# Performance work log

Measured on AMD Instinct MI355X. Metric: run time of the kernel, lower is better.

## Reference

```python
import jax, jax.numpy as jnp
import numpy as np

N_QUBITS = 8
DEPTH = 2
INPUT_DIM = 128
HIDDEN_DIM = 256
SEQ_LEN = 64
BATCH = 128
DIM = 2 ** N_QUBITS


def _rx(t):
    c = jnp.cos(0.5 * t).astype(jnp.complex64)
    s = (-1j * jnp.sin(0.5 * t)).astype(jnp.complex64)
    return jnp.stack([jnp.stack([c, s], -1), jnp.stack([s, c], -1)], -2)


def _ry(t):
    c = jnp.cos(0.5 * t).astype(jnp.complex64)
    s = jnp.sin(0.5 * t).astype(jnp.complex64)
    return jnp.stack([jnp.stack([c, -s], -1), jnp.stack([s, c], -1)], -2)


def _rz(t):
    e0 = jnp.exp(-0.5j * t).astype(jnp.complex64)
    e1 = jnp.exp(0.5j * t).astype(jnp.complex64)
    z = jnp.zeros_like(e0)
    return jnp.stack([jnp.stack([e0, z], -1), jnp.stack([z, e1], -1)], -2)


def _apply_1q(state, U, q):
    # state: (B, 2**n) complex; U: (2,2) shared or (B,2,2) per-sample
    b = state.shape[0]
    s = state.reshape(b, 2 ** q, 2, -1)
    if U.ndim == 2:
        s = jnp.einsum('ij,bljr->blir', U, s)
    else:
        s = jnp.einsum('bij,bljr->blir', U, s)
    return s.reshape(b, DIM)


def _apply_cnot(state, c, t):
    b = state.shape[0]
    s = state.reshape((b,) + (2,) * N_QUBITS)
    ac, at = 1 + c, 1 + t
    s0 = jnp.take(s, 0, axis=ac)
    s1 = jnp.take(s, 1, axis=ac)
    at2 = at - 1 if at > ac else at  # target axis shifts after slicing control axis
    s1 = jnp.flip(s1, axis=at2)
    s = jnp.stack([s0, s1], axis=ac)
    return s.reshape(b, DIM)


def _quantum_gate(x, params):
    # x: (B, n_qubits) data angles; params: (n_qubits, depth, 3) RX/RY/RZ angles
    b = x.shape[0]
    state = jnp.zeros((b, DIM), jnp.complex64).at[:, 0].set(1.0)
    for q in range(N_QUBITS):
        state = _apply_1q(state, _rx(x[:, q]), q)
    for d in range(DEPTH):
        for q in range(N_QUBITS):
            state = _apply_1q(state, _rx(params[q, d, 0]), q)
            state = _apply_1q(state, _ry(params[q, d, 1]), q)
            state = _apply_1q(state, _rz(params[q, d, 2]), q)
        for q in range(N_QUBITS - 1):
            state = _apply_cnot(state, q, q + 1)
        state = _apply_cnot(state, N_QUBITS - 1, 0)
    probs = state.real ** 2 + state.imag ** 2
    outs = []
    for q in range(N_QUBITS):  # <Z_q> = P(q=0) - P(q=1)
        p = probs.reshape(b, 2 ** q, 2, -1)
        outs.append(p[:, :, 0, :].sum((1, 2)) - p[:, :, 1, :].sum((1, 2)))
    return jnp.stack(outs, axis=1)


def _qlstm(inputs, Wf, bf, qf, Uf, cf, Wi, bi, qi, Ui, ci, Wg, bg, qg, Ug, cg, Wo, bo, qo, Uo, co):
    B = inputs.shape[1]
    h0 = jnp.zeros((B, HIDDEN_DIM), inputs.dtype)
    c0 = jnp.zeros((B, HIDDEN_DIM), inputs.dtype)

    def step(carry, x):
        hx, cx = carry
        comb = jnp.concatenate([x, hx], axis=1)

        def gate(W, b_, qp, U, c_):
            return _quantum_gate(comb @ W.T + b_, qp) @ U.T + c_

        f = jax.nn.sigmoid(gate(Wf, bf, qf, Uf, cf))
        i = jax.nn.sigmoid(gate(Wi, bi, qi, Ui, ci))
        g = jnp.tanh(gate(Wg, bg, qg, Ug, cg))
        o = jax.nn.sigmoid(gate(Wo, bo, qo, Uo, co))
        cx2 = f * cx + i * g
        hx2 = o * jnp.tanh(cx2)
        return (hx2, cx2), hx2

    (hx, cx), stacked = jax.lax.scan(step, (h0, c0), inputs)
    return stacked, hx, cx


def setup_inputs() -> dict:
    key = jax.random.key(0)
    ks = jax.random.split(key, 16)
    d = INPUT_DIM + HIDDEN_DIM
    inp = {"inputs": jax.random.normal(ks[0], (SEQ_LEN, BATCH, INPUT_DIM), jnp.float32)}
    k = 1
    for n in ("f", "i", "g", "o"):
        inp["W" + n] = jax.random.normal(ks[k], (N_QUBITS, d), jnp.float32) * 0.05; k += 1
        inp["b" + n] = jnp.zeros((N_QUBITS,), jnp.float32)
        inp["q" + n] = jax.random.normal(ks[k], (N_QUBITS, DEPTH, 3), jnp.float32) * 0.1; k += 1
        inp["U" + n] = jax.random.normal(ks[k], (HIDDEN_DIM, N_QUBITS), jnp.float32) * 0.05; k += 1
        inp["c" + n] = jnp.zeros((HIDDEN_DIM,), jnp.float32)
    return inp


def reference(inputs, Wf, bf, qf, Uf, cf, Wi, bi, qi, Ui, ci, Wg, bg, qg, Ug, cg, Wo, bo, qo, Uo, co):
    stacked, hx, cx = _qlstm(inputs, Wf, bf, qf, Uf, cf, Wi, bi, qi, Ui, ci,
                             Wg, bg, qg, Ug, cg, Wo, bo, qo, Uo, co)
    return stacked, (hx, cx)
```

## Files before the change

### kernel.cpp

```cpp
#include <hip/hip_runtime.h>
#include <math.h>

#define BB   128
#define TT   64
#define IND  128
#define HID  256
#define CD   384

struct C2 { float x, y; };
__device__ __forceinline__ C2 cmul(C2 a, C2 b) { return {a.x*b.x - a.y*b.y, a.x*b.y + a.y*b.x}; }
__device__ __forceinline__ C2 cadd(C2 a, C2 b) { return {a.x + b.x, a.y + b.y}; }
__device__ __forceinline__ C2 csub(C2 a, C2 b) { return {a.x - b.x, a.y - b.y}; }
__device__ __forceinline__ C2 conjc(C2 a) { return {a.x, -a.y}; }

struct Args {
    const float* x;
    const float* W[4];
    const float* bb[4];
    const float* qp[4];
    const float* Uo[4];
    const float* cb[4];
    float* out;
};

template<int CTRL>
__device__ __forceinline__ int dppmv(int v) {
    return __builtin_amdgcn_update_dpp(v, v, CTRL, 0xF, 0xF, false);
}

template<int M>
__device__ __forceinline__ float lx(float v) {
    int i = __float_as_int(v);
    if constexpr (M == 1)
        return __int_as_float(dppmv<0xB1>(i));
    else if constexpr (M == 2)
        return __int_as_float(dppmv<0x4E>(i));
    else if constexpr (M == 4) {
        int a = dppmv<0x104>(i);
        int b = dppmv<0x114>(i);
        return __int_as_float((threadIdx.x & 4) ? b : a);
    } else if constexpr (M == 8)
        return __int_as_float(dppmv<0x128>(i));
    else if constexpr (M == 16) {
#if __has_builtin(__builtin_amdgcn_permlane16_swap)
        auto r = __builtin_amdgcn_permlane16_swap(i, i, false, false);
        return __int_as_float((threadIdx.x & 16) ? r[0] : r[1]);
#else
        return __int_as_float(__builtin_amdgcn_ds_swizzle(i, 0x401F));
#endif
    } else {
#if __has_builtin(__builtin_amdgcn_permlane32_swap)
        auto r = __builtin_amdgcn_permlane32_swap(i, i, false, false);
        return __int_as_float((threadIdx.x & 32) ? r[0] : r[1]);
#else
        return __shfl_xor(v, 32);
#endif
    }
}

__device__ __forceinline__ float rfl(float v) {
    return __int_as_float(__builtin_amdgcn_readfirstlane(__float_as_int(v)));
}
__device__ __forceinline__ float bcast_lane(float v, int srclane) {
    return __int_as_float(__builtin_amdgcn_readlane(__float_as_int(v), srclane));
}
__device__ __forceinline__ float sigm(float x) {
    return __builtin_amdgcn_rcpf(1.f + __expf(-x));
}
__device__ __forceinline__ float tanh_fast(float x) {
    float e = __expf(2.f * x);
    return 1.f - 2.f * __builtin_amdgcn_rcpf(e + 1.f);
}
__device__ __forceinline__ float sgnx(float v, unsigned m) {
    return __int_as_float(__float_as_int(v) ^ (int)m);
}

template<int M>
__device__ __forceinline__ void gate_lane(float (&are)[4], float (&aim)[4], const float* u) {
#pragma unroll
    for (int r = 0; r < 4; ++r) {
        float px = lx<M>(are[r]);
        float py = lx<M>(aim[r]);
        float nx = u[0]*are[r] - u[1]*aim[r] + u[2]*px - u[3]*py;
        float ny = u[0]*aim[r] + u[1]*are[r] + u[2]*py + u[3]*px;
        are[r] = nx; aim[r] = ny;
    }
}

__device__ __forceinline__ void gate_pair2(float& a0x, float& a0y, float& a1x, float& a1y,
                                           float ax, float ay, float bx, float by) {
    float n0x = ax*a0x - ay*a0y + bx*a1x - by*a1y;
    float n0y = ax*a0y + ay*a0x + bx*a1y + by*a1x;
    float n1x = -bx*a0x - by*a0y + ax*a1x + ay*a1y;
    float n1y = -bx*a0y + by*a0x + ax*a1y - ay*a1x;
    a0x = n0x; a0y = n0y; a1x = n1x; a1y = n1y;
}

__global__ __launch_bounds__(256, 1) void qlstm_kernel(Args a) {
    const int b    = blockIdx.x;
    const int tid  = threadIdx.x;
    const int lane = tid & 63;
    const int wv   = tid >> 6;

    __shared__ float Ax[TT][32];
    __shared__ __align__(16) float hH[16][HID];
    __shared__ __align__(16) float4 uab[4][2][8];
    __shared__ __align__(16) float expL[32];

    const int a_ang = tid >> 3, p = tid & 7;
    const int g_ang = a_ang >> 3, q_ang = a_ang & 7;
    float whr[8][4];
    {
        const float* Wg = a.W[g_ang] + q_ang * CD + IND;
#pragma unroll
        for (int k = 0; k < 8; ++k) {
            int base = p * 32 + ((4 * (k + p)) & 31);
#pragma unroll
            for (int j = 0; j < 4; ++j) whr[k][j] = Wg[base + j];
        }
    }
    float ur[4][8], cbr[4];
#pragma unroll
    for (int g = 0; g < 4; ++g) {
#pragma unroll
        for (int k = 0; k < 8; ++k) ur[g][k] = a.Uo[g][tid * 8 + k];
        cbr[g] = a.cb[g][tid];
    }

    if (tid < 64) {
        int g = tid >> 4, d = (tid >> 3) & 1, q = tid & 7;
        const float* qp = a.qp[g] + q * 6 + d * 3;
        float s0, c0, s1, c1, s2, c2;
        sincosf(0.5f * qp[0], &s0, &c0);
        sincosf(0.5f * qp[1], &s1, &c1);
        sincosf(0.5f * qp[2], &s2, &c2);
        C2 aX{c0, 0.f}, bX{0.f, -s0};
        C2 aY{c1, 0.f}, bY{-s1, 0.f};
        C2 aB = csub(cmul(aY, aX), cmul(bY, conjc(bX)));
        C2 bB = cadd(cmul(aY, bX), cmul(bY, conjc(aX)));
        C2 aZ{c2, -s2};
        C2 al = cmul(aZ, aB), be = cmul(aZ, bB);
        uab[g][d][q] = make_float4(al.x, al.y, be.x, be.y);
    }

    for (int rep = 0; rep < 8; ++rep) {
        int idx = rep * 256 + tid;
        int t = idx >> 5, aa = idx & 31;
        int gg = aa >> 3, qq = aa & 7;
        const float4* w4 = (const float4*)(a.W[gg] + qq * CD);
        const float4* x4 = (const float4*)(a.x + (size_t)(t * BB + b) * IND);
        float acc = a.bb[gg][qq];
        for (int e = 0; e < IND / 4; ++e) {
            float4 xv = x4[e], wvv = w4[e];
            acc += xv.x * wvv.x + xv.y * wvv.y + xv.z * wvv.z + xv.w * wvv.w;
        }
        Ax[t][aa] = acc;
    }

    hH[15][tid] = 0.f;
    float creg = 0.f, h = 0.f;
    __syncthreads();

    float u0q[8][4];
#pragma unroll
    for (int q = 0; q < 8; ++q) {
        float4 u = uab[wv][0][q];
        u0q[q][0] = rfl(u.x); u0q[q][1] = rfl(u.y);
        u0q[q][2] = rfl(u.z); u0q[q][3] = rfl(u.w);
    }
    float gA[6][4];
#pragma unroll
    for (int qi = 0; qi < 6; ++qi) {
        float4 u = uab[wv][1][qi + 2];
        bool bit = (lane >> (5 - qi)) & 1;
        gA[qi][0] = u.x;
        gA[qi][1] = bit ? -u.y : u.y;
        gA[qi][2] = bit ? -u.z : u.z;
        gA[qi][3] = u.w;
    }
    float qr0[4], qr1[4];
    {
        float4 u0 = uab[wv][1][0], u1 = uab[wv][1][1];
        qr0[0] = rfl(u0.x); qr0[1] = rfl(u0.y); qr0[2] = rfl(u0.z); qr0[3] = rfl(u0.w);
        qr1[0] = rfl(u1.x); qr1[1] = rfl(u1.y); qr1[2] = rfl(u1.z); qr1[3] = rfl(u1.w);
    }

    const bool st3 = ((lane >> 4) ^ (lane >> 5)) & 1;
    const bool st4 = ((lane >> 3) ^ (lane >> 4)) & 1;
    const bool st5 = ((lane >> 2) ^ (lane >> 3)) & 1;
    const bool st6 = ((lane >> 1) ^ (lane >> 2)) & 1;
    const bool st7 = (lane ^ (lane >> 1)) & 1;
    const bool sp2 = (lane >> 5) & 1;
    const bool sp7 = lane & 1;

    unsigned sg0, sg2, sg3, sg4, sg5, sg6, sg7;
    {
        auto par31 = [](int v) -> unsigned { return (unsigned)(__popc(v) & 1) << 31; };
        sg0 = par31(lane & 63);
        sg2 = par31(lane & 32);
        sg3 = par31(lane & 48);
        sg4 = par31(lane & 56);
        sg5 = par31(lane & 60);
        sg6 = par31(lane & 62);
        sg7 = sg0;
    }

    for (int t = 0; t < TT; ++t) {
        const int rowPrev = (t + 15) & 15;
        const float* hrow = hH[rowPrev];
        float ac0 = 0.f, ac1 = 0.f;
#pragma unroll
        for (int k = 0; k < 8; ++k) {
            int base = p * 32 + ((4 * (k + p)) & 31);
            const float4 hv = *reinterpret_cast<const float4*>(&hrow[base]);
            if (k & 1) { ac1 += hv.x*whr[k][0] + hv.y*whr[k][1] + hv.z*whr[k][2] + hv.w*whr[k][3]; }
            else       { ac0 += hv.x*whr[k][0] + hv.y*whr[k][1] + hv.z*whr[k][2] + hv.w*whr[k][3]; }
        }
        float acc = ac0 + ac1;
        acc += lx<1>(acc);
        acc += lx<2>(acc);
        acc += lx<4>(acc);
        float ang = 0.5f * (acc + Ax[t][a_ang]);
        float cA = __cosf(ang), sA = __sinf(ang);
        float cs_c[8], cs_s[8];
#pragma unroll
        for (int q = 0; q < 8; ++q) {
            cs_c[q] = bcast_lane(cA, q * 8);
            cs_s[q] = bcast_lane(sA, q * 8);
        }

        float v0x[8], v0y[8], v1x[8], v1y[8];
#pragma unroll
        for (int q = 0; q < 8; ++q) {
            float c = cs_c[q], s = cs_s[q];
            float ax = u0q[q][0], ay = u0q[q][1], bx = u0q[q][2], by = u0q[q][3];
            v0x[q] =  ax*c + by*s;
            v0y[q] =  ay*c - bx*s;
            v1x[q] = -bx*c - ay*s;
            v1y[q] =  by*c - ax*s;
        }

        float are[4], aim[4];
        {
            C2 f3 = st3 ? C2{v1x[3], v1y[3]} : C2{v0x[3], v0y[3]};
            C2 f4 = st4 ? C2{v1x[4], v1y[4]} : C2{v0x[4], v0y[4]};
            C2 f5 = st5 ? C2{v1x[5], v1y[5]} : C2{v0x[5], v0y[5]};
            C2 f6 = st6 ? C2{v1x[6], v1y[6]} : C2{v0x[6], v0y[6]};
            C2 f7 = st7 ? C2{v1x[7], v1y[7]} : C2{v0x[7], v0y[7]};
            C2 common5 = cmul(cmul(cmul(f3, f4), cmul(f5, f6)), f7);
            C2 f2a = sp2 ? C2{v1x[2], v1y[2]} : C2{v0x[2], v0y[2]};
            C2 f2b = sp2 ? C2{v0x[2], v0y[2]} : C2{v1x[2], v1y[2]};
            C2 c2a = cmul(common5, f2a);
            C2 c2b = cmul(common5, f2b);
            C2 f0a = sp7 ? C2{v1x[0], v1y[0]} : C2{v0x[0], v0y[0]};
            C2 f0b = sp7 ? C2{v0x[0], v0y[0]} : C2{v1x[0], v1y[0]};
            C2 f1a = sp7 ? C2{v1x[1], v1y[1]} : C2{v0x[1], v0y[1]};
            C2 f1b = sp7 ? C2{v0x[1], v0y[1]} : C2{v1x[1], v1y[1]};
            C2 uu = cmul(f1a, f0a);
            C2 m1 = cmul(f1b, f0a);
            C2 ww = cmul(f1b, f0b);
            C2 m2 = cmul(f1a, f0b);
            C2 a0 = cmul(c2a, uu), a1 = cmul(c2b, m1);
            C2 a2 = cmul(c2a, ww), a3 = cmul(c2b, m2);
            are[0] = a0.x; aim[0] = a0.y;
            are[1] = a1.x; aim[1] = a1.y;
            are[2] = a2.x; aim[2] = a2.y;
            are[3] = a3.x; aim[3] = a3.y;
        }

        gate_pair2(are[0], aim[0], are[2], aim[2], qr0[0], qr0[1], qr0[2], qr0[3]);
        gate_pair2(are[1], aim[1], are[3], aim[3], qr0[0], qr0[1], qr0[2], qr0[3]);
        gate_pair2(are[0], aim[0], are[1], aim[1], qr1[0], qr1[1], qr1[2], qr1[3]);
        gate_pair2(are[2], aim[2], are[3], aim[3], qr1[0], qr1[1], qr1[2], qr1[3]);
        gate_lane<32>(are, aim, gA[0]);
        gate_lane<16>(are, aim, gA[1]);
        gate_lane< 8>(are, aim, gA[2]);
        gate_lane< 4>(are, aim, gA[3]);
        gate_lane< 2>(are, aim, gA[4]);
        gate_lane< 1>(are, aim, gA[5]);

        float pr[4];
#pragma unroll
        for (int r = 0; r < 4; ++r) pr[r] = are[r]*are[r] + aim[r]*aim[r];
        float Bc = pr[0] - pr[1] + pr[2] - pr[3];
        float Dc = pr[0] - pr[1] - pr[2] + pr[3];
        float z[8];
        z[0] = sgnx(Bc, sg0);
        z[1] = Dc;
        z[2] = sgnx(Dc, sg2);
        z[3] = sgnx(Dc, sg3);
        z[4] = sgnx(Dc, sg4);
        z[5] = sgnx(Dc, sg5);
        z[6] = sgnx(Dc, sg6);
        z[7] = sgnx(Dc, sg7);
        float w4a[4];
#pragma unroll
        for (int j = 0; j < 8; ++j) z[j] += lx<1>(z[j]);
#pragma unroll
        for (int j = 0; j < 4; ++j) w4a[j] = (lane & 1) ? z[j + 4] : z[j];
        float w2a[2];
#pragma unroll
        for (int j = 0; j < 4; ++j) w4a[j] += lx<2>(w4a[j]);
#pragma unroll
        for (int j = 0; j < 2; ++j) w2a[j] = (lane & 2) ? w4a[j + 2] : w4a[j];
        w2a[0] += lx<4>(w2a[0]);
        w2a[1] += lx<4>(w2a[1]);
        float wz = (lane & 4) ? w2a[1] : w2a[0];
        wz += lx<8>(wz);
        wz += lx<16>(wz);
        wz += lx<32>(wz);
        if (lane < 8)
            expL[wv*8 + (((lane & 1) << 2) | (lane & 2) | ((lane >> 2) & 1))] = wz;
        __syncthreads();

        const float4* eL = (const float4*)expL;
        float og[4];
#pragma unroll
        for (int g = 0; g < 4; ++g) {
            float4 e0 = eL[g*2], e1 = eL[g*2 + 1];
            og[g] = cbr[g]
                  + e0.x*ur[g][0] + e0.y*ur[g][1] + e0.z*ur[g][2] + e0.w*ur[g][3]
                  + e1.x*ur[g][4] + e1.y*ur[g][5] + e1.z*ur[g][6] + e1.w*ur[g][7];
        }
        float fg = sigm(og[0]);
        float ig = sigm(og[1]);
        float gg = tanh_fast(og[2]);
        float oo = sigm(og[3]);
        creg = fg * creg + ig * gg;
        h = oo * tanh_fast(creg);

        hH[t & 15][tid] = h;
        if ((t & 15) == 15) {
            int t0 = t - 15;
#pragma unroll
            for (int r = 0; r < 16; ++r)
                a.out[(size_t)((t0 + r) * BB + b) * HID + tid] = hH[r][tid];
        }
        __syncthreads();
    }

    a.out[(size_t)TT * BB * HID + (size_t)b * HID + tid] = h;
    a.out[(size_t)TT * BB * HID + (size_t)BB * HID + (size_t)b * HID + tid] = creg;
}

extern "C" void kernel_launch(void* const* d_in, const int* in_sizes, int n_in,
                              void* d_out, int out_size, void* d_ws, size_t ws_size,
                              hipStream_t stream) {
    (void)in_sizes; (void)n_in; (void)out_size; (void)d_ws; (void)ws_size;
    Args ar;
    ar.x = (const float*)d_in[0];
    for (int g = 0; g < 4; ++g) {
        ar.W[g]  = (const float*)d_in[1 + 5 * g];
        ar.bb[g] = (const float*)d_in[2 + 5 * g];
        ar.qp[g] = (const float*)d_in[3 + 5 * g];
        ar.Uo[g] = (const float*)d_in[4 + 5 * g];
        ar.cb[g] = (const float*)d_in[5 + 5 * g];
    }
    ar.out = (float*)d_out;
    qlstm_kernel<<<dim3(BB), dim3(256), 0, stream>>>(ar);
}
```

Measured before the change: 160.8 us.

## Vectorize per-step quantum simulation and LSTM math with packed float2 ops

Rewrites the recurrent step's arithmetic using two-wide float vectors so the compiler can emit packed FP32 instructions (v_pk_fma/mul) for the hidden projection, the single-qubit gate applications, the product-state build and the output projection. The expectation reduction is also restructured to reduce all eight qubit sums with full butterfly shuffles instead of the select-and-halve scheme, changing the expL layout to [qubit][gate]. This aims to cut VALU instruction count on the serial per-timestep critical path. The trade-off is more cross-lane shuffles in the reduction, plus possible extra swizzle/move instructions for the lane-swapped operands.

```diff
diff --git a/kernel.cpp b/kernel.cpp
--- a/kernel.cpp
+++ b/kernel.cpp
@@ -7,11 +7,16 @@
 #define HID  256
 #define CD   384
 
+typedef float v2f __attribute__((ext_vector_type(2)));
+
 struct C2 { float x, y; };
 __device__ __forceinline__ C2 cmul(C2 a, C2 b) { return {a.x*b.x - a.y*b.y, a.x*b.y + a.y*b.x}; }
 __device__ __forceinline__ C2 cadd(C2 a, C2 b) { return {a.x + b.x, a.y + b.y}; }
 __device__ __forceinline__ C2 csub(C2 a, C2 b) { return {a.x - b.x, a.y - b.y}; }
 __device__ __forceinline__ C2 conjc(C2 a) { return {a.x, -a.y}; }
+
+__device__ __forceinline__ v2f pk(float a, float b) { v2f r; r.x = a; r.y = b; return r; }
+__device__ __forceinline__ v2f swp(v2f v) { return __builtin_shufflevector(v, v, 1, 0); }
 
 struct Args {
     const float* x;
@@ -57,6 +62,10 @@
 #endif
     }
 }
+template<int M>
+__device__ __forceinline__ v2f lx2(v2f v) {
+    return pk(lx<M>(v.x), lx<M>(v.y));
+}
 
 __device__ __forceinline__ float rfl(float v) {
     return __int_as_float(__builtin_amdgcn_readfirstlane(__float_as_int(v)));
@@ -76,24 +85,15 @@
 }
 
 template<int M>
-__device__ __forceinline__ void gate_lane(float (&are)[4], float (&aim)[4], const float* u) {
-#pragma unroll
-    for (int r = 0; r < 4; ++r) {
-        float px = lx<M>(are[r]);
-        float py = lx<M>(aim[r]);
-        float nx = u[0]*are[r] - u[1]*aim[r] + u[2]*px - u[3]*py;
-        float ny = u[0]*aim[r] + u[1]*are[r] + u[2]*py + u[3]*px;
-        are[r] = nx; aim[r] = ny;
-    }
-}
-
-__device__ __forceinline__ void gate_pair2(float& a0x, float& a0y, float& a1x, float& a1y,
-                                           float ax, float ay, float bx, float by) {
-    float n0x = ax*a0x - ay*a0y + bx*a1x - by*a1y;
-    float n0y = ax*a0y + ay*a0x + bx*a1y + by*a1x;
-    float n1x = -bx*a0x - by*a0y + ax*a1x + ay*a1y;
-    float n1y = -bx*a0y + by*a0x + ax*a1y - ay*a1x;
-    a0x = n0x; a0y = n0y; a1x = n1x; a1y = n1y;
+__device__ __forceinline__ void gate_lane_pk(v2f& xe01, v2f& xi01, v2f& xe23, v2f& xi23,
+                                             float u0, float u1, float u2, float u3) {
+    v2f px0 = lx2<M>(xe01), py0 = lx2<M>(xi01);
+    v2f px2 = lx2<M>(xe23), py2 = lx2<M>(xi23);
+    v2f ne0 = u0*xe01 - u1*xi01 + u2*px0 - u3*py0;
+    v2f ni0 = u0*xi01 + u1*xe01 + u2*py0 + u3*px0;
+    v2f ne2 = u0*xe23 - u1*xi23 + u2*px2 - u3*py2;
+    v2f ni2 = u0*xi23 + u1*xe23 + u2*py2 + u3*px2;
+    xe01 = ne0; xi01 = ni0; xe23 = ne2; xi23 = ni2;
 }
 
 __global__ __launch_bounds__(256, 1) void qlstm_kernel(Args a) {
@@ -109,23 +109,24 @@
 
     const int a_ang = tid >> 3, p = tid & 7;
     const int g_ang = a_ang >> 3, q_ang = a_ang & 7;
-    float whr[8][4];
+    v2f whr2[8][2];
     {
         const float* Wg = a.W[g_ang] + q_ang * CD + IND;
 #pragma unroll
         for (int k = 0; k < 8; ++k) {
             int base = p * 32 + ((4 * (k + p)) & 31);
-#pragma unroll
-            for (int j = 0; j < 4; ++j) whr[k][j] = Wg[base + j];
-        }
-    }
-    float ur[4][8], cbr[4];
-#pragma unroll
-    for (int g = 0; g < 4; ++g) {
-#pragma unroll
-        for (int k = 0; k < 8; ++k) ur[g][k] = a.Uo[g][tid * 8 + k];
-        cbr[g] = a.cb[g][tid];
-    }
+            whr2[k][0] = pk(Wg[base + 0], Wg[base + 1]);
+            whr2[k][1] = pk(Wg[base + 2], Wg[base + 3]);
+        }
+    }
+    v2f ur2a[8], ur2b[8], cb2a, cb2b;
+#pragma unroll
+    for (int k = 0; k < 8; ++k) {
+        ur2a[k] = pk(a.Uo[0][tid * 8 + k], a.Uo[1][tid * 8 + k]);
+        ur2b[k] = pk(a.Uo[2][tid * 8 + k], a.Uo[3][tid * 8 + k]);
+    }
+    cb2a = pk(a.cb[0][tid], a.cb[1][tid]);
+    cb2b = pk(a.cb[2][tid], a.cb[3][tid]);
 
     if (tid < 64) {
         int g = tid >> 4, d = (tid >> 3) & 1, q = tid & 7;
@@ -161,12 +162,15 @@
     float creg = 0.f, h = 0.f;
     __syncthreads();
 
-    float u0q[8][4];
+    v2f pA[8], pB[8], pC[8], pD[8];
 #pragma unroll
     for (int q = 0; q < 8; ++q) {
         float4 u = uab[wv][0][q];
-        u0q[q][0] = rfl(u.x); u0q[q][1] = rfl(u.y);
-        u0q[q][2] = rfl(u.z); u0q[q][3] = rfl(u.w);
+        float ax = rfl(u.x), ay = rfl(u.y), bx = rfl(u.z), by = rfl(u.w);
+        pA[q] = pk(ax, -bx);
+        pB[q] = pk(by, -ay);
+        pC[q] = pk(ay, by);
+        pD[q] = pk(-bx, -ax);
     }
     float gA[6][4];
 #pragma unroll
@@ -178,11 +182,17 @@
         gA[qi][2] = bit ? -u.z : u.z;
         gA[qi][3] = u.w;
     }
-    float qr0[4], qr1[4];
+    float q0ax, q0ay, q0bx, q0by;
+    float q1ax, q1by;
+    v2f q1aym, q1ayp, q1bxm;
     {
         float4 u0 = uab[wv][1][0], u1 = uab[wv][1][1];
-        qr0[0] = rfl(u0.x); qr0[1] = rfl(u0.y); qr0[2] = rfl(u0.z); qr0[3] = rfl(u0.w);
-        qr1[0] = rfl(u1.x); qr1[1] = rfl(u1.y); qr1[2] = rfl(u1.z); qr1[3] = rfl(u1.w);
+        q0ax = rfl(u0.x); q0ay = rfl(u0.y); q0bx = rfl(u0.z); q0by = rfl(u0.w);
+        q1ax = rfl(u1.x); q1by = rfl(u1.w);
+        float ay = rfl(u1.y), bx = rfl(u1.z);
+        q1aym = pk(-ay, ay);
+        q1ayp = pk(ay, -ay);
+        q1bxm = pk(bx, -bx);
     }
 
     const bool st3 = ((lane >> 4) ^ (lane >> 5)) & 1;
@@ -208,15 +218,14 @@
     for (int t = 0; t < TT; ++t) {
         const int rowPrev = (t + 15) & 15;
         const float* hrow = hH[rowPrev];
-        float ac0 = 0.f, ac1 = 0.f;
+        v2f acc2 = pk(0.f, 0.f);
 #pragma unroll
         for (int k = 0; k < 8; ++k) {
             int base = p * 32 + ((4 * (k + p)) & 31);
             const float4 hv = *reinterpret_cast<const float4*>(&hrow[base]);
-            if (k & 1) { ac1 += hv.x*whr[k][0] + hv.y*whr[k][1] + hv.z*whr[k][2] + hv.w*whr[k][3]; }
-            else       { ac0 += hv.x*whr[k][0] + hv.y*whr[k][1] + hv.z*whr[k][2] + hv.w*whr[k][3]; }
-        }
-        float acc = ac0 + ac1;
+            acc2 = acc2 + pk(hv.x, hv.y) * whr2[k][0] + pk(hv.z, hv.w) * whr2[k][1];
+        }
+        float acc = acc2.x + acc2.y;
         acc += lx<1>(acc);
         acc += lx<2>(acc);
         acc += lx<4>(acc);
@@ -229,103 +238,98 @@
             cs_s[q] = bcast_lane(sA, q * 8);
         }
 
-        float v0x[8], v0y[8], v1x[8], v1y[8];
+        v2f Vx[8], Vy[8];
 #pragma unroll
         for (int q = 0; q < 8; ++q) {
-            float c = cs_c[q], s = cs_s[q];
-            float ax = u0q[q][0], ay = u0q[q][1], bx = u0q[q][2], by = u0q[q][3];
-            v0x[q] =  ax*c + by*s;
-            v0y[q] =  ay*c - bx*s;
-            v1x[q] = -bx*c - ay*s;
-            v1y[q] =  by*c - ax*s;
-        }
-
-        float are[4], aim[4];
+            Vx[q] = pA[q] * cs_c[q] + pB[q] * cs_s[q];
+            Vy[q] = pC[q] * cs_c[q] + pD[q] * cs_s[q];
+        }
+
+        v2f xe01, xi01, xe23, xi23;
         {
-            C2 f3 = st3 ? C2{v1x[3], v1y[3]} : C2{v0x[3], v0y[3]};
-            C2 f4 = st4 ? C2{v1x[4], v1y[4]} : C2{v0x[4], v0y[4]};
-            C2 f5 = st5 ? C2{v1x[5], v1y[5]} : C2{v0x[5], v0y[5]};
-            C2 f6 = st6 ? C2{v1x[6], v1y[6]} : C2{v0x[6], v0y[6]};
-            C2 f7 = st7 ? C2{v1x[7], v1y[7]} : C2{v0x[7], v0y[7]};
-            C2 common5 = cmul(cmul(cmul(f3, f4), cmul(f5, f6)), f7);
-            C2 f2a = sp2 ? C2{v1x[2], v1y[2]} : C2{v0x[2], v0y[2]};
-            C2 f2b = sp2 ? C2{v0x[2], v0y[2]} : C2{v1x[2], v1y[2]};
-            C2 c2a = cmul(common5, f2a);
-            C2 c2b = cmul(common5, f2b);
-            C2 f0a = sp7 ? C2{v1x[0], v1y[0]} : C2{v0x[0], v0y[0]};
-            C2 f0b = sp7 ? C2{v0x[0], v0y[0]} : C2{v1x[0], v1y[0]};
-            C2 f1a = sp7 ? C2{v1x[1], v1y[1]} : C2{v0x[1], v0y[1]};
-            C2 f1b = sp7 ? C2{v0x[1], v0y[1]} : C2{v1x[1], v1y[1]};
-            C2 uu = cmul(f1a, f0a);
-            C2 m1 = cmul(f1b, f0a);
-            C2 ww = cmul(f1b, f0b);
-            C2 m2 = cmul(f1a, f0b);
-            C2 a0 = cmul(c2a, uu), a1 = cmul(c2b, m1);
-            C2 a2 = cmul(c2a, ww), a3 = cmul(c2b, m2);
-            are[0] = a0.x; aim[0] = a0.y;
-            are[1] = a1.x; aim[1] = a1.y;
-            are[2] = a2.x; aim[2] = a2.y;
-            are[3] = a3.x; aim[3] = a3.y;
-        }
-
-        gate_pair2(are[0], aim[0], are[2], aim[2], qr0[0], qr0[1], qr0[2], qr0[3]);
-        gate_pair2(are[1], aim[1], are[3], aim[3], qr0[0], qr0[1], qr0[2], qr0[3]);
-        gate_pair2(are[0], aim[0], are[1], aim[1], qr1[0], qr1[1], qr1[2], qr1[3]);
-        gate_pair2(are[2], aim[2], are[3], aim[3], qr1[0], qr1[1], qr1[2], qr1[3]);
-        gate_lane<32>(are, aim, gA[0]);
-        gate_lane<16>(are, aim, gA[1]);
-        gate_lane< 8>(are, aim, gA[2]);
-        gate_lane< 4>(are, aim, gA[3]);
-        gate_lane< 2>(are, aim, gA[4]);
-        gate_lane< 1>(are, aim, gA[5]);
-
-        float pr[4];
-#pragma unroll
-        for (int r = 0; r < 4; ++r) pr[r] = are[r]*are[r] + aim[r]*aim[r];
-        float Bc = pr[0] - pr[1] + pr[2] - pr[3];
-        float Dc = pr[0] - pr[1] - pr[2] + pr[3];
-        float z[8];
-        z[0] = sgnx(Bc, sg0);
-        z[1] = Dc;
-        z[2] = sgnx(Dc, sg2);
-        z[3] = sgnx(Dc, sg3);
-        z[4] = sgnx(Dc, sg4);
-        z[5] = sgnx(Dc, sg5);
-        z[6] = sgnx(Dc, sg6);
-        z[7] = sgnx(Dc, sg7);
-        float w4a[4];
-#pragma unroll
-        for (int j = 0; j < 8; ++j) z[j] += lx<1>(z[j]);
-#pragma unroll
-        for (int j = 0; j < 4; ++j) w4a[j] = (lane & 1) ? z[j + 4] : z[j];
-        float w2a[2];
-#pragma unroll
-        for (int j = 0; j < 4; ++j) w4a[j] += lx<2>(w4a[j]);
-#pragma unroll
-        for (int j = 0; j < 2; ++j) w2a[j] = (lane & 2) ? w4a[j + 2] : w4a[j];
-        w2a[0] += lx<4>(w2a[0]);
-        w2a[1] += lx<4>(w2a[1]);
-        float wz = (lane & 4) ? w2a[1] : w2a[0];
-        wz += lx<8>(wz);
-        wz += lx<16>(wz);
-        wz += lx<32>(wz);
-        if (lane < 8)
-            expL[wv*8 + (((lane & 1) << 2) | (lane & 2) | ((lane >> 2) & 1))] = wz;
+            C2 f3{ st3 ? Vx[3].y : Vx[3].x, st3 ? Vy[3].y : Vy[3].x };
+            C2 f4{ st4 ? Vx[4].y : Vx[4].x, st4 ? Vy[4].y : Vy[4].x };
+            C2 f5{ st5 ? Vx[5].y : Vx[5].x, st5 ? Vy[5].y : Vy[5].x };
+            C2 f6{ st6 ? Vx[6].y : Vx[6].x, st6 ? Vy[6].y : Vy[6].x };
+            C2 f7{ st7 ? Vx[7].y : Vx[7].x, st7 ? Vy[7].y : Vy[7].x };
+            C2 c5 = cmul(cmul(cmul(f3, f4), cmul(f5, f6)), f7);
+            v2f f2re = sp2 ? swp(Vx[2]) : Vx[2];
+            v2f f2im = sp2 ? swp(Vy[2]) : Vy[2];
+            v2f c2re = c5.x * f2re - c5.y * f2im;
+            v2f c2im = c5.x * f2im + c5.y * f2re;
+            v2f f1re = sp7 ? swp(Vx[1]) : Vx[1];
+            v2f f1im = sp7 ? swp(Vy[1]) : Vy[1];
+            float f0ax = sp7 ? Vx[0].y : Vx[0].x, f0ay = sp7 ? Vy[0].y : Vy[0].x;
+            float f0bx = sp7 ? Vx[0].x : Vx[0].y, f0by = sp7 ? Vy[0].x : Vy[0].y;
+            v2f uure = f1re * f0ax - f1im * f0ay;
+            v2f uuim = f1re * f0ay + f1im * f0ax;
+            v2f s1re = swp(f1re), s1im = swp(f1im);
+            v2f wwre = s1re * f0bx - s1im * f0by;
+            v2f wwim = s1re * f0by + s1im * f0bx;
+            xe01 = c2re * uure - c2im * uuim;
+            xi01 = c2re * uuim + c2im * uure;
+            xe23 = c2re * wwre - c2im * wwim;
+            xi23 = c2re * wwim + c2im * wwre;
+        }
+
+        {
+            v2f ne01 = q0ax*xe01 - q0ay*xi01 + q0bx*xe23 - q0by*xi23;
+            v2f ni01 = q0ax*xi01 + q0ay*xe01 + q0bx*xi23 + q0by*xe23;
+            v2f ne23 = -q0bx*xe01 - q0by*xi01 + q0ax*xe23 + q0ay*xi23;
+            v2f ni23 = -q0bx*xi01 + q0by*xe01 + q0ax*xi23 - q0ay*xe23;
+            xe01 = ne01; xi01 = ni01; xe23 = ne23; xi23 = ni23;
+        }
+        {
+            v2f se01 = swp(xe01), si01 = swp(xi01);
+            v2f se23 = swp(xe23), si23 = swp(xi23);
+            v2f ne01 = q1ax*xe01 + q1aym*xi01 + q1bxm*se01 - q1by*si01;
+            v2f ni01 = q1ax*xi01 + q1ayp*xe01 + q1bxm*si01 + q1by*se01;
+            v2f ne23 = q1ax*xe23 + q1aym*xi23 + q1bxm*se23 - q1by*si23;
+            v2f ni23 = q1ax*xi23 + q1ayp*xe23 + q1bxm*si23 + q1by*se23;
+            xe01 = ne01; xi01 = ni01; xe23 = ne23; xi23 = ni23;
+        }
+        gate_lane_pk<32>(xe01, xi01, xe23, xi23, gA[0][0], gA[0][1], gA[0][2], gA[0][3]);
+        gate_lane_pk<16>(xe01, xi01, xe23, xi23, gA[1][0], gA[1][1], gA[1][2], gA[1][3]);
+        gate_lane_pk< 8>(xe01, xi01, xe23, xi23, gA[2][0], gA[2][1], gA[2][2], gA[2][3]);
+        gate_lane_pk< 4>(xe01, xi01, xe23, xi23, gA[3][0], gA[3][1], gA[3][2], gA[3][3]);
+        gate_lane_pk< 2>(xe01, xi01, xe23, xi23, gA[4][0], gA[4][1], gA[4][2], gA[4][3]);
+        gate_lane_pk< 1>(xe01, xi01, xe23, xi23, gA[5][0], gA[5][1], gA[5][2], gA[5][3]);
+
+        v2f pr01 = xe01 * xe01 + xi01 * xi01;
+        v2f pr23 = xe23 * xe23 + xi23 * xi23;
+        float pr0 = pr01.x, pr1 = pr01.y, pr2 = pr23.x, pr3 = pr23.y;
+        float Bc = pr0 - pr1 + pr2 - pr3;
+        float Dc = pr0 - pr1 - pr2 + pr3;
+        v2f zA = pk(sgnx(Bc, sg0), Dc);
+        v2f zB = pk(sgnx(Dc, sg2), sgnx(Dc, sg3));
+        v2f zC = pk(sgnx(Dc, sg4), sgnx(Dc, sg5));
+        v2f zD = pk(sgnx(Dc, sg6), sgnx(Dc, sg7));
+        zA = zA + lx2<1>(zA);  zB = zB + lx2<1>(zB);  zC = zC + lx2<1>(zC);  zD = zD + lx2<1>(zD);
+        zA = zA + lx2<2>(zA);  zB = zB + lx2<2>(zB);  zC = zC + lx2<2>(zC);  zD = zD + lx2<2>(zD);
+        zA = zA + lx2<4>(zA);  zB = zB + lx2<4>(zB);  zC = zC + lx2<4>(zC);  zD = zD + lx2<4>(zD);
+        zA = zA + lx2<8>(zA);  zB = zB + lx2<8>(zB);  zC = zC + lx2<8>(zC);  zD = zD + lx2<8>(zD);
+        zA = zA + lx2<16>(zA); zB = zB + lx2<16>(zB); zC = zC + lx2<16>(zC); zD = zD + lx2<16>(zD);
+        zA = zA + lx2<32>(zA); zB = zB + lx2<32>(zB); zC = zC + lx2<32>(zC); zD = zD + lx2<32>(zD);
+        if (lane == 0) {
+            expL[0*4 + wv] = zA.x; expL[1*4 + wv] = zA.y;
+            expL[2*4 + wv] = zB.x; expL[3*4 + wv] = zB.y;
+            expL[4*4 + wv] = zC.x; expL[5*4 + wv] = zC.y;
+            expL[6*4 + wv] = zD.x; expL[7*4 + wv] = zD.y;
+        }
         __syncthreads();
 
-        const float4* eL = (const float4*)expL;
-        float og[4];
-#pragma unroll
-        for (int g = 0; g < 4; ++g) {
-            float4 e0 = eL[g*2], e1 = eL[g*2 + 1];
-            og[g] = cbr[g]
-                  + e0.x*ur[g][0] + e0.y*ur[g][1] + e0.z*ur[g][2] + e0.w*ur[g][3]
-                  + e1.x*ur[g][4] + e1.y*ur[g][5] + e1.z*ur[g][6] + e1.w*ur[g][7];
-        }
-        float fg = sigm(og[0]);
-        float ig = sigm(og[1]);
-        float gg = tanh_fast(og[2]);
-        float oo = sigm(og[3]);
+        const float4* eL4 = (const float4*)expL;
+        v2f og2a = cb2a, og2b = cb2b;
+#pragma unroll
+        for (int k = 0; k < 8; ++k) {
+            float4 e4 = eL4[k];
+            og2a = og2a + pk(e4.x, e4.y) * ur2a[k];
+            og2b = og2b + pk(e4.z, e4.w) * ur2b[k];
+        }
+        float fg = sigm(og2a.x);
+        float ig = sigm(og2a.y);
+        float gg = tanh_fast(og2b.x);
+        float oo = sigm(og2b.y);
         creg = fg * creg + ig * gg;
         h = oo * tanh_fast(creg);
 
```

Result: faster. 131.3 us (median of 2 runs) (-18.3%).
